# Kernel optimization log

Measured on AMD Instinct MI355X. Metric: run time of the kernel, lower is better.

The kernel has to match this reference:

```python
import jax, jax.numpy as jnp
import numpy as np

R_DIM, R2_DIM, MIX, IN_DIM, HID = 128, 64, 32, 512, 256
B, T = 256, 16
MAX_ITER = 12
LR_R, LR_R2 = 0.1, 0.1
LMDA_R, LMDA_R2 = 0.01, 0.01
SPAT_W, TEMP_W = 1.0, 1.0
LN_EPS = 1e-6


def _soft_thresh(r, lmda):
    # non-negative proximal L1 step, as in the source soft_thresholding
    return jax.nn.relu(jnp.abs(r) - lmda) * jnp.sign(r)


def setup_inputs() -> dict:
    key = jax.random.key(0)
    ks = jax.random.split(key, 8)

    def xavier(k, shape):
        std = (2.0 / (shape[0] + shape[-1])) ** 0.5
        return std * jax.random.normal(k, shape, dtype=jnp.float32)

    return {
        'X': jax.random.normal(ks[0], (B, T, IN_DIM), dtype=jnp.float32),
        'dec_W': xavier(ks[1], (R_DIM, IN_DIM)),
        'dec_b': jnp.zeros((IN_DIM,), jnp.float32),
        'temporal': xavier(ks[2], (MIX, R_DIM * R_DIM)),
        'h1_W': xavier(ks[3], (R2_DIM, HID)),
        'h1_b': jnp.zeros((HID,), jnp.float32),
        'ln_s': jnp.ones((HID,), jnp.float32),
        'ln_b': jnp.zeros((HID,), jnp.float32),
        'h2_W': xavier(ks[4], (HID, HID)),
        'h2_b': jnp.zeros((HID,), jnp.float32),
        'h3_W': xavier(ks[5], (HID, MIX)),
        'h3_b': jnp.zeros((MIX,), jnp.float32),
    }


def _hypernet(r2, h1_W, h1_b, ln_s, ln_b, h2_W, h2_b, h3_W, h3_b):
    x = r2 @ h1_W + h1_b
    mu = jnp.mean(x, axis=-1, keepdims=True)
    var = jnp.var(x, axis=-1, keepdims=True)
    x = (x - mu) * jax.lax.rsqrt(var + LN_EPS) * ln_s + ln_b  # LayerNorm
    x = jax.nn.elu(x)
    x = x @ h2_W + h2_b
    x = x @ h3_W + h3_b
    return jax.nn.relu(x)  # mixture weights w: (B, MIX)


def _forward(X, dec_W, dec_b, temporal, h1_W, h1_b, ln_s, ln_b, h2_W, h2_b, h3_W, h3_b):
    hp = (h1_W, h1_b, ln_s, ln_b, h2_W, h2_b, h3_W, h3_b)
    Vk = temporal.reshape(MIX, R_DIM, R_DIM)

    def decode(r):
        return r @ dec_W + dec_b  # linear spatial decoder (MSE branch)

    def temp_pred(r_prev, r2):
        w = _hypernet(r2, *hp)                       # (B, MIX)
        V = jnp.einsum('bm,mij->bij', w, Vk)         # (B, R, R)
        return jnp.einsum('bij,bj->bi', V, r_prev)   # r_hat: (B, R)

    def time_step(carry, x_t):
        r_prev, r2 = carry

        def energy(r, r2_):
            r_hat = temp_pred(r_prev, r2_)
            spat = jnp.sum((decode(r) - x_t) ** 2)
            temp = jnp.sum((r - r_hat) ** 2)
            return SPAT_W * spat + TEMP_W * temp

        grad_fn = jax.grad(energy, argnums=(0, 1))

        def ista(c, _):
            r, r2_ = c
            gr, gr2 = grad_fn(r, r2_)
            r = _soft_thresh(r - LR_R * gr, LR_R * LMDA_R)
            r2_ = _soft_thresh(r2_ - LR_R2 * gr2, LR_R2 * LMDA_R2)
            return (r, r2_), None

        r0 = temp_pred(r_prev, r2)  # warm start from temporal prediction
        (r, r2), _ = jax.lax.scan(ista, (r0, r2), None, length=MAX_ITER)

        r_hat = temp_pred(r_prev, r2)
        spat_rhat = jnp.mean(jnp.sum((decode(r_hat) - x_t) ** 2, axis=-1))
        spat_rbar = jnp.mean(jnp.sum((decode(r) - x_t) ** 2, axis=-1))
        temp_loss = jnp.mean(jnp.sum((r - r_hat) ** 2, axis=-1))
        return (r, r2), jnp.stack([spat_rhat, spat_rbar, temp_loss])

    r_init = jnp.zeros((X.shape[0], R_DIM), X.dtype)
    r2_init = jnp.zeros((X.shape[0], R2_DIM), X.dtype)
    (r_fin, r2_fin), losses = jax.lax.scan(
        time_step, (r_init, r2_init), jnp.swapaxes(X, 0, 1))
    return jnp.mean(losses, axis=0), r_fin, r2_fin


def reference(X, dec_W, dec_b, temporal, h1_W, h1_b, ln_s, ln_b, h2_W, h2_b, h3_W, h3_b):
    return _forward(X, dec_W, dec_b, temporal, h1_W, h1_b, ln_s, ln_b,
                    h2_W, h2_b, h3_W, h3_b)
```

## Files before the change

kernel.cpp:

```cpp
#include <hip/hip_runtime.h>
#include <cstdint>
#include <cstddef>

#define R_DIM   128
#define R2_DIM  64
#define MIX     32
#define IN_DIM  512
#define HID     256
#define B_SZ    256
#define T_SZ    16
#define MAX_IT  12

#define OFF_G    0
#define OFF_U    24576
#define OFF_SX   548864
#define OFF_FLAG 552960
#define OFF_LOSS 552961

__device__ __forceinline__ float softt(float v, float lam) {
  float a = fabsf(v) - lam;
  return a > 0.f ? (v > 0.f ? a : -a) : 0.f;
}

__device__ __forceinline__ float rdlane(float v, int lane) {
  int i = __builtin_amdgcn_readlane(__float_as_int(v), lane);
  return __int_as_float(i);
}

__device__ __forceinline__ float wsum_all(float v) {
#pragma unroll
  for (int off = 32; off; off >>= 1) v += __shfl_xor(v, off, 64);
  return v;
}

__device__ __forceinline__ float wsum(float v) {
#pragma unroll
  for (int off = 32; off; off >>= 1) v += __shfl_down(v, off, 64);
  return v;
}

__device__ __forceinline__ float pairsum32(float pm) {
  float a = pm, b = pm;
  asm volatile("v_permlane32_swap_b32 %0, %1" : "+v"(a), "+v"(b));
  return a + b;
}

__device__ void ensure_c_dev(int l, const float* __restrict__ T2, float* cS,
                             int* cstL, const float* rpL) {
  if (cstL[0]) return;
  for (int p = l; p < MIX * R_DIM; p += 64) {
    const float* row = T2 + (size_t)p * R_DIM;
    float acc = 0.f;
    for (int j4 = 0; j4 < R_DIM / 4; j4++) {
      float4 w4 = *(const float4*)(row + j4 * 4);
      float4 r4 = *(const float4*)(rpL + j4 * 4);
      acc += w4.x * r4.x + w4.y * r4.y + w4.z * r4.z + w4.w * r4.w;
    }
    cS[(p >> 7) * 129 + (p & 127)] = acc;
  }
  if (l == 0) cstL[0] = 1;
}

__device__ __noinline__ float2 rhat_cold(int l, const float* __restrict__ T2,
                                         float* cS, int* cstL,
                                         const float* rpL, const float* wL) {
  ensure_c_dev(l, T2, cS, cstL, rpL);
  float a0 = 0.f, a1 = 0.f;
#pragma unroll
  for (int m4 = 0; m4 < 8; m4++) {
    float4 w4 = *(const float4*)&wL[m4 * 4];
    int mb = m4 * 4;
    a0 += w4.x * cS[(mb + 0) * 129 + l] + w4.y * cS[(mb + 1) * 129 + l] +
          w4.z * cS[(mb + 2) * 129 + l] + w4.w * cS[(mb + 3) * 129 + l];
    a1 += w4.x * cS[(mb + 0) * 129 + 64 + l] + w4.y * cS[(mb + 1) * 129 + 64 + l] +
          w4.z * cS[(mb + 2) * 129 + 64 + l] + w4.w * cS[(mb + 3) * 129 + 64 + l];
  }
  return make_float2(a0, a1);
}

__device__ __noinline__ int hyp_fwd_cold(
    int l, float r2v, int zr2,
    const float* __restrict__ h1W, const float* __restrict__ h1b,
    const float* __restrict__ lns, const float* __restrict__ lnb,
    const float* __restrict__ h2W, const float* __restrict__ h2b,
    const float* __restrict__ h3W, const float* __restrict__ h3b,
    float* aL, float* xhL, float* x2L, float* wL, float* rstdL) {
  float x1[4];
#pragma unroll
  for (int q = 0; q < 4; q++) x1[q] = h1b[l + 64 * q];
  if (!zr2) {
    for (int k = 0; k < R2_DIM; k++) {
      float rk = rdlane(r2v, k);
      if (rk != 0.f) {
#pragma unroll
        for (int q = 0; q < 4; q++) x1[q] += rk * h1W[k * HID + l + 64 * q];
      }
    }
  }
  float s1 = x1[0] + x1[1] + x1[2] + x1[3];
  float s2 = x1[0] * x1[0] + x1[1] * x1[1] + x1[2] * x1[2] + x1[3] * x1[3];
  s1 = wsum_all(s1); s2 = wsum_all(s2);
  float mu = s1 * (1.f / HID);
  float var = s2 * (1.f / HID) - mu * mu;
  float rstd = rsqrtf(var + 1e-6f);
  if (l == 0) rstdL[0] = rstd;
  bool anz = false;
#pragma unroll
  for (int q = 0; q < 4; q++) {
    float xh = (x1[q] - mu) * rstd;
    xhL[l + 64 * q] = xh;
    float y = xh * lns[l + 64 * q] + lnb[l + 64 * q];
    float a = (y > 0.f) ? y : expm1f(y);
    aL[l + 64 * q] = a;
    anz |= (a != 0.f);
  }
  bool za = (__ballot(anz) == 0ull);
  float x2[4];
#pragma unroll
  for (int q = 0; q < 4; q++) x2[q] = h2b[l + 64 * q];
  if (!za) {
    for (int k4 = 0; k4 < HID / 4; k4++) {
      float4 a4 = *(const float4*)&aL[k4 * 4];
#pragma unroll
      for (int c = 0; c < 4; c++) {
        float ac = (&a4.x)[c];
        int k = k4 * 4 + c;
#pragma unroll
        for (int q = 0; q < 4; q++) x2[q] += ac * h2W[(size_t)k * HID + l + 64 * q];
      }
    }
  }
  bool x2nz = false;
#pragma unroll
  for (int q = 0; q < 4; q++) { x2L[l + 64 * q] = x2[q]; x2nz |= (x2[q] != 0.f); }
  bool zx2 = (__ballot(x2nz) == 0ull);
  int m = l & 31, kh = l >> 5;
  float p = 0.f;
  if (!zx2) {
    for (int kk = 0; kk < 128; kk++) {
      int k = kh * 128 + kk;
      p += x2L[k] * h3W[k * MIX + m];
    }
  }
  p += __shfl_xor(p, 32, 64);
  float wv = 0.f;
  if (l < 32) { wv = fmaxf(h3b[l] + p, 0.f); wL[l] = wv; }
  return (__ballot(wv != 0.f) == 0ull) ? 1 : 0;
}

__device__ __noinline__ float2 hyp_bwd_cold(
    int l, float r2v, int zw,
    const float* __restrict__ T2,
    const float* __restrict__ h1W, const float* __restrict__ lns,
    const float* __restrict__ h2W, const float* __restrict__ h3W,
    float* cS, int* cstL, const float* rpL, const float* eL,
    const float* aL, const float* xhL, const float* wL,
    float* dx3L, float* dx2L, float* dx1L, const float* rstdL) {
  bool zd3 = true;
  if (!zw) {
    ensure_c_dev(l, T2, cS, cstL, rpL);
    int m = l & 31, ih = l >> 5;
    float p = 0.f;
    for (int ii = 0; ii < 64; ii++) {
      int i = ih * 64 + ii;
      p += eL[i] * cS[m * 129 + i];
    }
    p += __shfl_xor(p, 32, 64);
    float d3 = 0.f;
    if (l < 32) { d3 = (wL[l] > 0.f) ? (-2.f * p) : 0.f; dx3L[l] = d3; }
    zd3 = (__ballot(d3 != 0.f) == 0ull);
  }
  float g = 0.f;
  if (!zd3) {
    float rstd = rstdL[0];
    float dx2[4] = {0.f, 0.f, 0.f, 0.f};
#pragma unroll
    for (int m4 = 0; m4 < 8; m4++) {
      float4 d4 = *(const float4*)&dx3L[m4 * 4];
#pragma unroll
      for (int q = 0; q < 4; q++) {
        const float* r3 = h3W + (size_t)(l + 64 * q) * MIX + m4 * 4;
        dx2[q] += d4.x * r3[0] + d4.y * r3[1] + d4.z * r3[2] + d4.w * r3[3];
      }
    }
#pragma unroll
    for (int q = 0; q < 4; q++) dx2L[l + 64 * q] = dx2[q];
    float dxh[4];
    float s1 = 0.f, s2 = 0.f;
#pragma unroll
    for (int q = 0; q < 4; q++) {
      float da = 0.f;
      const float* row = h2W + (size_t)(l + 64 * q) * HID;
      for (int k4 = 0; k4 < HID / 4; k4++) {
        float4 w4 = *(const float4*)(row + k4 * 4);
        float4 d4 = *(const float4*)&dx2L[k4 * 4];
        da += w4.x * d4.x + w4.y * d4.y + w4.z * d4.z + w4.w * d4.w;
      }
      float a = aL[l + 64 * q];
      float dy = da * (a > 0.f ? 1.f : (a + 1.f));
      dxh[q] = dy * lns[l + 64 * q];
      s1 += dxh[q]; s2 += dxh[q] * xhL[l + 64 * q];
    }
    s1 = wsum_all(s1); s2 = wsum_all(s2);
#pragma unroll
    for (int q = 0; q < 4; q++) {
      float dx1 = rstd * (dxh[q] - s1 * (1.f / HID) - xhL[l + 64 * q] * (s2 * (1.f / HID)));
      dx1L[l + 64 * q] = dx1;
    }
    const float* row1 = h1W + (size_t)l * HID;
    for (int j4 = 0; j4 < HID / 4; j4++) {
      float4 w4 = *(const float4*)(row1 + j4 * 4);
      float4 d4 = *(const float4*)&dx1L[j4 * 4];
      g += w4.x * d4.x + w4.y * d4.y + w4.z * d4.z + w4.w * d4.w;
    }
  }
  float r2n = softt(r2v - 0.1f * g, 0.001f);
  int fl = 0;
  if (__ballot(r2n != r2v) != 0ull) fl |= 1;
  if (__ballot(r2n != 0.f) == 0ull) fl |= 2;
  return make_float2(r2n, __int_as_float(fl));
}

__global__ __launch_bounds__(256) void k_prep(const float* __restrict__ X,
                                              const float* __restrict__ decb,
                                              const float* __restrict__ decW,
                                              const float* __restrict__ h1W,
                                              const float* __restrict__ h1b,
                                              const float* __restrict__ lns,
                                              const float* __restrict__ lnb,
                                              const float* __restrict__ h2W,
                                              const float* __restrict__ h2b,
                                              const float* __restrict__ h3W,
                                              const float* __restrict__ h3b,
                                              float* __restrict__ ws,
                                              float* __restrict__ out) {
  __shared__ __align__(16) float As[8][IN_DIM];
  __shared__ float Wsp[128][65];
  __shared__ float scr[256];
  __shared__ __align__(16) float aF[HID], xhF[HID], x2F[HID];
  __shared__ __align__(16) float wF[MIX];
  __shared__ float rsF[1];
  float* G = ws + OFF_G;
  float* U = ws + OFF_U;
  float* SX = ws + OFF_SX;
  const int tid = threadIdx.x;
  const int bx = blockIdx.x;

  if (bx == 528) {
    if (tid < 64) {
      int z = hyp_fwd_cold(tid, 0.f, 1, h1W, h1b, lns, lnb, h2W, h2b, h3W, h3b,
                           aF, xhF, x2F, wF, rsF);
      if (tid == 0) ((int*)(ws + OFF_FLAG))[0] = z;
    }
    return;
  }
  const bool isG = (bx >= 512);

  if (bx == 0 && tid < 3) out[tid] = 0.f;
  if (bx == 0 && tid < 48) ws[OFF_LOSS + tid] = 0.f;

  {
    int g = tid >> 5;
    int f0 = tid & 31;
    if (!isG) {
      int row0 = bx * 8;
      float p = 0.f;
#pragma unroll
      for (int q = 0; q < 4; q++) {
        int f4 = f0 + 32 * q;
        float4 xv = *reinterpret_cast<const float4*>(X + (size_t)(row0 + g) * IN_DIM + f4 * 4);
        float4 bv = *reinterpret_cast<const float4*>(decb + f4 * 4);
        float4 v = make_float4(xv.x - bv.x, xv.y - bv.y, xv.z - bv.z, xv.w - bv.w);
        *reinterpret_cast<float4*>(&As[g][f4 * 4]) = v;
        p += v.x * v.x + v.y * v.y + v.z * v.z + v.w * v.w;
      }
      scr[tid] = p;
    } else {
      int row0 = (bx - 512) * 8;
#pragma unroll
      for (int q = 0; q < 4; q++) {
        int f4 = f0 + 32 * q;
        float4 v = *reinterpret_cast<const float4*>(decW + (size_t)(row0 + g) * IN_DIM + f4 * 4);
        *reinterpret_cast<float4*>(&As[g][f4 * 4]) = v;
      }
    }
  }
  __syncthreads();
  if (!isG && tid < 8) {
    float s = 0.f;
#pragma unroll
    for (int q = 0; q < 32; q++) s += scr[tid * 32 + q];
    SX[bx * 8 + tid] = s;
  }

  const int j = tid & 127;
  const int gh = tid >> 7;
  float acc[4] = {0.f, 0.f, 0.f, 0.f};

  for (int kp = 0; kp < 8; kp++) {
    __syncthreads();
#pragma unroll
    for (int pass = 0; pass < 8; pass++) {
      int row = pass * 16 + (tid >> 4);
      int kk = (tid & 15) * 4;
      float4 v = *reinterpret_cast<const float4*>(decW + (size_t)row * IN_DIM + kp * 64 + kk);
      Wsp[row][kk + 0] = v.x; Wsp[row][kk + 1] = v.y;
      Wsp[row][kk + 2] = v.z; Wsp[row][kk + 3] = v.w;
    }
    __syncthreads();
    float wreg[64];
#pragma unroll
    for (int kk = 0; kk < 64; kk++) wreg[kk] = Wsp[j][kk];
#pragma unroll
    for (int gi = 0; gi < 4; gi++) {
      int gg = gh * 4 + gi;
      float a = acc[gi];
#pragma unroll
      for (int k4 = 0; k4 < 16; k4++) {
        float4 a4 = *reinterpret_cast<const float4*>(&As[gg][kp * 64 + k4 * 4]);
        a += a4.x * wreg[k4 * 4 + 0] + a4.y * wreg[k4 * 4 + 1] +
             a4.z * wreg[k4 * 4 + 2] + a4.w * wreg[k4 * 4 + 3];
      }
      acc[gi] = a;
    }
  }

  if (!isG) {
    int row0 = bx * 8;
#pragma unroll
    for (int gi = 0; gi < 4; gi++)
      U[(size_t)(row0 + gh * 4 + gi) * R_DIM + j] = acc[gi];
  } else {
    int row0 = (bx - 512) * 8;
#pragma unroll
    for (int gi = 0; gi < 4; gi++) {
      int rr = row0 + gh * 4 + gi;
      float gv = -0.2f * acc[gi];
      if (rr == j) gv += 0.8f;
      G[(size_t)rr * R_DIM + j] = gv;
    }
  }
}

__global__ __launch_bounds__(256, 4) void k_ista(float* __restrict__ ws,
                                                 float* __restrict__ out) {
  if (((const int*)(ws + OFF_FLAG))[0] == 0) return;
  __shared__ __align__(16) float rbuf[2][R_DIM];
  __shared__ float scr[8];

  const int tid = threadIdx.x;
  const int w = tid >> 6;
  const int l6 = tid & 63;
  const int i = (w << 5) + (l6 & 31);
  const int kh = l6 >> 5;
  const int bt = blockIdx.x;
  const int b = bt >> 4;
  const int t = bt & 15;
  const float* Gg = ws + OFF_G;
  const float* Ug = ws + OFF_U;

  float Ga[64];
#pragma unroll
  for (int kk = 0; kk < 64; kk++)
    Ga[kk] = Gg[(size_t)(kh * 64 + kk) * R_DIM + i];

  const float u = Ug[(size_t)bt * R_DIM + i];
  const float u02 = 0.2f * u;

  auto mvhalf = [&](const float* vptr) {
    const float* vp = vptr + (kh << 6);
    float p0 = 0.f, p1 = 0.f, p2 = 0.f, p3 = 0.f;
#pragma unroll
    for (int k4 = 0; k4 < 16; k4++) {
      float4 v4 = *reinterpret_cast<const float4*>(vp + k4 * 4);
      p0 += v4.x * Ga[k4 * 4 + 0];
      p1 += v4.y * Ga[k4 * 4 + 1];
      p2 += v4.z * Ga[k4 * 4 + 2];
      p3 += v4.w * Ga[k4 * 4 + 3];
    }
    float pm = (p0 + p1) + (p2 + p3);
    return pairsum32(pm);
  };

  float r = softt(u02, 0.001f);
  if (kh == 0) rbuf[1][i] = r;
  __syncthreads();
#pragma unroll 1
  for (int it = 1; it < MAX_IT; it++) {
    float mv = mvhalf(rbuf[it & 1]);
    r = softt(mv + u02, 0.001f);
    if (kh == 0) rbuf[(it & 1) ^ 1][i] = r;
    __syncthreads();
  }
  float mvf = mvhalf(rbuf[0]);
  float gb = 0.8f * r - mvf;
  float l1 = (kh == 0) ? (r * (5.f * gb) - 2.f * r * u) : 0.f;
  float l2 = (kh == 0) ? (r * r) : 0.f;
  l1 = wsum(l1); l2 = wsum(l2);
  if (l6 == 0) { scr[w * 2 + 0] = l1; scr[w * 2 + 1] = l2; }
  __syncthreads();
  if (tid == 0) {
    float s1 = scr[0] + scr[2] + scr[4] + scr[6];
    float s2 = scr[1] + scr[3] + scr[5] + scr[7];
    float sx = ws[OFF_SX + bt];
    float* loss = ws + OFF_LOSS;
    atomicAdd(&loss[0 * 16 + t], sx);
    atomicAdd(&loss[1 * 16 + t], s1 + sx);
    atomicAdd(&loss[2 * 16 + t], s2);
  }
  if (t == T_SZ - 1 && kh == 0) out[3 + b * R_DIM + i] = r;
  if (t == 0 && w == 0) out[3 + B_SZ * R_DIM + b * R2_DIM + l6] = 0.f;
}

__global__ void k_fin(const float* __restrict__ ws, float* __restrict__ out) {
  if (((const int*)(ws + OFF_FLAG))[0] == 0) return;
  int k = threadIdx.x;
  if (k < 3) {
    float s = 0.f;
#pragma unroll
    for (int t = 0; t < 16; t++) s += ws[OFF_LOSS + k * 16 + t];
    out[k] = s * (1.f / (B_SZ * T_SZ));
  }
}

__global__ __launch_bounds__(256, 1) void k_main(
    float* __restrict__ ws, const float* __restrict__ T2,
    const float* __restrict__ h1W, const float* __restrict__ h1b,
    const float* __restrict__ lns, const float* __restrict__ lnb,
    const float* __restrict__ h2W, const float* __restrict__ h2b,
    const float* __restrict__ h3W, const float* __restrict__ h3b,
    float* __restrict__ out) {
  if (((const int*)(ws + OFF_FLAG))[0] != 0) return;
  __shared__ __align__(16) float rbuf[2][R_DIM];
  __shared__ __align__(16) float rhL[R_DIM];
  __shared__ __align__(16) float cS[MIX * 129];
  __shared__ __align__(16) float aL[HID];
  __shared__ __align__(16) float xhL[HID];
  __shared__ __align__(16) float x2L[HID];
  __shared__ __align__(16) float dx1L[HID];
  __shared__ __align__(16) float dx2L[HID];
  __shared__ __align__(16) float wL[MIX];
  __shared__ __align__(16) float dx3L[MIX];
  __shared__ __align__(16) float eL[R_DIM];
  __shared__ __align__(16) float rpL[R_DIM];
  __shared__ float rstdL[1];
  __shared__ int cstL[1];
  __shared__ int flagL[1];

  const int tid = threadIdx.x;
  const int w = tid >> 6;
  const int l6 = tid & 63;
  const int i = (w << 5) + (l6 & 31);
  const int kh = l6 >> 5;
  const int b = blockIdx.x;
  const float* Gg = ws + OFF_G;
  const float* Ug = ws + OFF_U;
  const float* SXg = ws + OFF_SX;

  float r2v = 0.f;
  bool zr2 = true, rhv;

  if (w == 0) {
    int z = hyp_fwd_cold(l6, 0.f, 1, h1W, h1b, lns, lnb, h2W, h2b, h3W, h3b,
                         aL, xhL, x2L, wL, rstdL);
    if (l6 == 0) flagL[0] = z;
  }
  __syncthreads();
  bool zw = flagL[0] != 0;

  float Ga[64];
#pragma unroll
  for (int kk = 0; kk < 64; kk++)
    Ga[kk] = Gg[(size_t)(kh * 64 + kk) * R_DIM + i];

  float rOwn = 0.f;
  float lc0 = 0.f, lc1 = 0.f, lc2 = 0.f, sxa = 0.f;

  auto mvhalf = [&](const float* vptr) {
    const float* vp = vptr + (kh << 6);
    float p0 = 0.f, p1 = 0.f, p2 = 0.f, p3 = 0.f;
#pragma unroll
    for (int k4 = 0; k4 < 16; k4++) {
      float4 v4 = *reinterpret_cast<const float4*>(vp + k4 * 4);
      p0 += v4.x * Ga[k4 * 4 + 0];
      p1 += v4.y * Ga[k4 * 4 + 1];
      p2 += v4.z * Ga[k4 * 4 + 2];
      p3 += v4.w * Ga[k4 * 4 + 3];
    }
    float pm = (p0 + p1) + (p2 + p3);
    return pm + __shfl_xor(pm, 32, 64);
  };

  float rh_own = 0.f;
  auto refresh_rh = [&]() {
    if (zw) { rh_own = 0.f; return; }
    __syncthreads();
    if (w == 0) {
      float2 rr = rhat_cold(l6, T2, cS, cstL, rpL, wL);
      rhL[l6] = rr.x; rhL[64 + l6] = rr.y;
    }
    __syncthreads();
    rh_own = rhL[i];
  };

  float un = Ug[(size_t)(b * T_SZ) * R_DIM + i];
  float sxn = SXg[b * T_SZ];

#pragma unroll 1
  for (int t = 0; t < T_SZ; t++) {
    float u = un, sxv = sxn;
    if (t < T_SZ - 1) {
      un = Ug[(size_t)(b * T_SZ + t + 1) * R_DIM + i];
      sxn = SXg[b * T_SZ + t + 1];
    }
    float u02 = 0.2f * u;
    if (kh == 0) rpL[i] = rOwn;
    if (tid == 0) cstL[0] = 0;
    refresh_rh();
    rhv = true;
    rOwn = rh_own;
    __syncthreads();
    if (kh == 0) rbuf[0][i] = rOwn;
    __syncthreads();
    bool rzero = zw;
#pragma unroll 1
    for (int it = 0; it < MAX_IT; it++) {
      if (!rhv) { refresh_rh(); rhv = true; }
      float mv = 0.f;
      if (!rzero) mv = mvhalf(rbuf[it & 1]);
      rzero = false;
      float rNew = softt(mv + 0.2f * rh_own + u02, 0.001f);
      if (kh == 0) {
        eL[i] = rOwn - rh_own;
        rbuf[(it & 1) ^ 1][i] = rNew;
      }
      rOwn = rNew;
      __syncthreads();
      if (!(zw && zr2)) {
        if (w == 0) {
          float2 br = hyp_bwd_cold(l6, r2v, zw ? 1 : 0, T2, h1W, lns, h2W, h3W,
                                   cS, cstL, rpL, eL, aL, xhL, wL,
                                   dx3L, dx2L, dx1L, rstdL);
          r2v = br.x;
          if (l6 == 0) flagL[0] = __float_as_int(br.y);
        }
        __syncthreads();
        int fl = flagL[0];
        zr2 = (fl & 2) != 0;
        if (fl & 1) {
          if (w == 0) {
            int z = hyp_fwd_cold(l6, r2v, zr2 ? 1 : 0, h1W, h1b, lns, lnb,
                                 h2W, h2b, h3W, h3b, aL, xhL, x2L, wL, rstdL);
            if (l6 == 0) flagL[0] = z;
          }
          __syncthreads();
          zw = flagL[0] != 0;
          rhv = false;
        }
      }
    }
    if (!rhv) { refresh_rh(); rhv = true; }
    {
      float mv = mvhalf(rbuf[MAX_IT & 1]);
      float gb = 0.8f * rOwn - mv;
      if (kh == 0) lc1 += rOwn * (5.f * gb) - 2.f * rOwn * u;
      if (zw) {
        if (kh == 0) lc2 += rOwn * rOwn;
      } else {
        float mvh = mvhalf(rhL);
        float gh = 0.8f * rh_own - mvh;
        if (kh == 0) {
          lc0 += rh_own * (5.f * gh) - 2.f * rh_own * u;
          float d = rOwn - rh_own;
          lc2 += d * d;
        }
      }
      if (tid == 0) sxa += sxv;
    }
  }

  const float inv = 1.f / (B_SZ * T_SZ);
  float t0 = wsum(lc0), t1 = wsum(lc1), t2 = wsum(lc2);
  if (l6 == 0) {
    float s = (w == 0) ? sxa : 0.f;
    atomicAdd(&out[0], (t0 + s) * inv);
    atomicAdd(&out[1], (t1 + s) * inv);
    atomicAdd(&out[2], t2 * inv);
  }
  if (kh == 0) out[3 + b * R_DIM + i] = rOwn;
  if (w == 0) out[3 + B_SZ * R_DIM + b * R2_DIM + l6] = r2v;
}

extern "C" void kernel_launch(void* const* d_in, const int* in_sizes, int n_in,
                              void* d_out, int out_size, void* d_ws, size_t ws_size,
                              hipStream_t stream) {
  const float* X = (const float*)d_in[0];
  const float* decW = (const float*)d_in[1];
  const float* decb = (const float*)d_in[2];
  const float* temporal = (const float*)d_in[3];
  const float* h1W = (const float*)d_in[4];
  const float* h1b = (const float*)d_in[5];
  const float* lns = (const float*)d_in[6];
  const float* lnb = (const float*)d_in[7];
  const float* h2W = (const float*)d_in[8];
  const float* h2b = (const float*)d_in[9];
  const float* h3W = (const float*)d_in[10];
  const float* h3b = (const float*)d_in[11];
  float* ws = (float*)d_ws;
  float* out = (float*)d_out;

  k_prep<<<529, 256, 0, stream>>>(X, decb, decW, h1W, h1b, lns, lnb,
                                  h2W, h2b, h3W, h3b, ws, out);
  k_main<<<B_SZ, 256, 0, stream>>>(ws, temporal, h1W, h1b, lns, lnb,
                                   h2W, h2b, h3W, h3b, out);
  k_ista<<<B_SZ * T_SZ, 256, 0, stream>>>(ws, out);
  k_fin<<<1, 64, 0, stream>>>(ws, out);
}
```

Before: 202.0 us.

## Process two (b,t) problems per ISTA block with each lane holding two G columns

The ISTA kernel now handles two batch-time problems per block, and each thread keeps two 64-element slices of the G matrix in registers. All 64 lanes of a wave now produce a useful output, where before only half did after the pair reduction. This removes the idle half-lanes in the final stage and halves the number of blocks and G reloads. In exchange, register use per thread doubles (128 floats for G), so the launch bound is lowered to 2 waves per SIMD, which reduces occupancy.

```diff
diff --git a/kernel.cpp b/kernel.cpp
--- a/kernel.cpp
+++ b/kernel.cpp
@@ -342,74 +342,81 @@
   }
 }
 
-__global__ __launch_bounds__(256, 4) void k_ista(float* __restrict__ ws,
+__global__ __launch_bounds__(256, 2) void k_ista(float* __restrict__ ws,
                                                  float* __restrict__ out) {
   if (((const int*)(ws + OFF_FLAG))[0] == 0) return;
-  __shared__ __align__(16) float rbuf[2][R_DIM];
+  __shared__ __align__(16) float rbuf[2][2][R_DIM];
   __shared__ float scr[8];
 
   const int tid = threadIdx.x;
-  const int w = tid >> 6;
+  const int half = tid >> 7;
+  const int wv = tid >> 6;
+  const int wbt = wv & 1;
   const int l6 = tid & 63;
-  const int i = (w << 5) + (l6 & 31);
+  const int p = (wbt << 5) + (l6 & 31);
   const int kh = l6 >> 5;
-  const int bt = blockIdx.x;
+  const int iown = p + (kh << 6);
+  const int bt = blockIdx.x * 2 + half;
   const int b = bt >> 4;
   const int t = bt & 15;
   const float* Gg = ws + OFF_G;
   const float* Ug = ws + OFF_U;
 
-  float Ga[64];
-#pragma unroll
-  for (int kk = 0; kk < 64; kk++)
-    Ga[kk] = Gg[(size_t)(kh * 64 + kk) * R_DIM + i];
-
-  const float u = Ug[(size_t)bt * R_DIM + i];
+  float Ga0[64], Ga1[64];
+#pragma unroll
+  for (int kk = 0; kk < 64; kk++) {
+    const float* row = Gg + (size_t)(kh * 64 + kk) * R_DIM;
+    Ga0[kk] = row[p];
+    Ga1[kk] = row[p + 64];
+  }
+
+  const float u = Ug[(size_t)bt * R_DIM + iown];
   const float u02 = 0.2f * u;
 
-  auto mvhalf = [&](const float* vptr) {
-    const float* vp = vptr + (kh << 6);
-    float p0 = 0.f, p1 = 0.f, p2 = 0.f, p3 = 0.f;
+  auto mvown = [&](const float* vbase) {
+    const float* vp = vbase + (kh << 6);
+    float s0a = 0.f, s0b = 0.f, s1a = 0.f, s1b = 0.f;
 #pragma unroll
     for (int k4 = 0; k4 < 16; k4++) {
       float4 v4 = *reinterpret_cast<const float4*>(vp + k4 * 4);
-      p0 += v4.x * Ga[k4 * 4 + 0];
-      p1 += v4.y * Ga[k4 * 4 + 1];
-      p2 += v4.z * Ga[k4 * 4 + 2];
-      p3 += v4.w * Ga[k4 * 4 + 3];
-    }
-    float pm = (p0 + p1) + (p2 + p3);
-    return pairsum32(pm);
+      s0a += v4.x * Ga0[k4 * 4 + 0] + v4.y * Ga0[k4 * 4 + 1];
+      s0b += v4.z * Ga0[k4 * 4 + 2] + v4.w * Ga0[k4 * 4 + 3];
+      s1a += v4.x * Ga1[k4 * 4 + 0] + v4.y * Ga1[k4 * 4 + 1];
+      s1b += v4.z * Ga1[k4 * 4 + 2] + v4.w * Ga1[k4 * 4 + 3];
+    }
+    float mv0 = pairsum32(s0a + s0b);
+    float mv1 = pairsum32(s1a + s1b);
+    return kh ? mv1 : mv0;
   };
 
   float r = softt(u02, 0.001f);
-  if (kh == 0) rbuf[1][i] = r;
+  rbuf[half][1][iown] = r;
   __syncthreads();
 #pragma unroll 1
   for (int it = 1; it < MAX_IT; it++) {
-    float mv = mvhalf(rbuf[it & 1]);
+    float mv = mvown(&rbuf[half][it & 1][0]);
     r = softt(mv + u02, 0.001f);
-    if (kh == 0) rbuf[(it & 1) ^ 1][i] = r;
+    rbuf[half][(it & 1) ^ 1][iown] = r;
     __syncthreads();
   }
-  float mvf = mvhalf(rbuf[0]);
+  float mvf = mvown(&rbuf[half][0][0]);
   float gb = 0.8f * r - mvf;
-  float l1 = (kh == 0) ? (r * (5.f * gb) - 2.f * r * u) : 0.f;
-  float l2 = (kh == 0) ? (r * r) : 0.f;
+  float l1 = r * (5.f * gb) - 2.f * r * u;
+  float l2 = r * r;
   l1 = wsum(l1); l2 = wsum(l2);
-  if (l6 == 0) { scr[w * 2 + 0] = l1; scr[w * 2 + 1] = l2; }
+  if (l6 == 0) { scr[wv * 2 + 0] = l1; scr[wv * 2 + 1] = l2; }
   __syncthreads();
-  if (tid == 0) {
-    float s1 = scr[0] + scr[2] + scr[4] + scr[6];
-    float s2 = scr[1] + scr[3] + scr[5] + scr[7];
+  if ((tid & 127) == 0) {
+    float s1 = scr[half * 4 + 0] + scr[half * 4 + 2];
+    float s2 = scr[half * 4 + 1] + scr[half * 4 + 3];
     float sx = ws[OFF_SX + bt];
     float* loss = ws + OFF_LOSS;
     atomicAdd(&loss[0 * 16 + t], sx);
     atomicAdd(&loss[1 * 16 + t], s1 + sx);
     atomicAdd(&loss[2 * 16 + t], s2);
   }
-  if (t == T_SZ - 1 && kh == 0) out[3 + b * R_DIM + i] = r;
-  if (t == 0 && w == 0) out[3 + B_SZ * R_DIM + b * R2_DIM + l6] = 0.f;
+  if (t == T_SZ - 1) out[3 + b * R_DIM + iown] = r;
+  if (t == 0 && wbt == 0) out[3 + B_SZ * R_DIM + b * R2_DIM + l6] = 0.f;
 }
 
 __global__ void k_fin(const float* __restrict__ ws, float* __restrict__ out) {
@@ -613,6 +620,6 @@
                                   h2W, h2b, h3W, h3b, ws, out);
   k_main<<<B_SZ, 256, 0, stream>>>(ws, temporal, h1W, h1b, lns, lnb,
                                    h2W, h2b, h3W, h3b, out);
-  k_ista<<<B_SZ * T_SZ, 256, 0, stream>>>(ws, out);
+  k_ista<<<B_SZ * T_SZ / 2, 256, 0, stream>>>(ws, out);
   k_fin<<<1, 64, 0, stream>>>(ws, out);
 }
```

Measured after the change: 207.9 us. +2.9%, slower.

## Fold final loss reduction into k_ista and stream decW directly in prep GEMM

Applied to the files above, without the earlier changes.

Removes the separate k_fin launch: the last k_ista block, found with a global atomic counter after a threadfence, sums the per-timestep losses and writes the outputs. The prep GEMM no longer stages decW tiles through padded shared memory with two barriers per tile; each thread instead reads its decW row with float4 global loads. An empty asm barrier pins the G coefficients in registers in k_ista. This saves one kernel launch and the shared-memory staging and syncs, in exchange for uncoalesced row-strided global loads and an atomic counter.

```diff
diff --git a/kernel.cpp b/kernel.cpp
--- a/kernel.cpp
+++ b/kernel.cpp
@@ -16,6 +16,7 @@
 #define OFF_SX   548864
 #define OFF_FLAG 552960
 #define OFF_LOSS 552961
+#define OFF_CNT  553012
 
 __device__ __forceinline__ float softt(float v, float lam) {
   float a = fabsf(v) - lam;
@@ -235,7 +236,6 @@
                                               float* __restrict__ ws,
                                               float* __restrict__ out) {
   __shared__ __align__(16) float As[8][IN_DIM];
-  __shared__ float Wsp[128][65];
   __shared__ float scr[256];
   __shared__ __align__(16) float aF[HID], xhF[HID], x2F[HID];
   __shared__ __align__(16) float wF[MIX];
@@ -258,6 +258,7 @@
 
   if (bx == 0 && tid < 3) out[tid] = 0.f;
   if (bx == 0 && tid < 48) ws[OFF_LOSS + tid] = 0.f;
+  if (bx == 0 && tid == 48) ((int*)(ws + OFF_CNT))[0] = 0;
 
   {
     int g = tid >> 5;
@@ -296,32 +297,15 @@
   const int j = tid & 127;
   const int gh = tid >> 7;
   float acc[4] = {0.f, 0.f, 0.f, 0.f};
-
-  for (int kp = 0; kp < 8; kp++) {
-    __syncthreads();
-#pragma unroll
-    for (int pass = 0; pass < 8; pass++) {
-      int row = pass * 16 + (tid >> 4);
-      int kk = (tid & 15) * 4;
-      float4 v = *reinterpret_cast<const float4*>(decW + (size_t)row * IN_DIM + kp * 64 + kk);
-      Wsp[row][kk + 0] = v.x; Wsp[row][kk + 1] = v.y;
-      Wsp[row][kk + 2] = v.z; Wsp[row][kk + 3] = v.w;
-    }
-    __syncthreads();
-    float wreg[64];
-#pragma unroll
-    for (int kk = 0; kk < 64; kk++) wreg[kk] = Wsp[j][kk];
+  const float* wrow = decW + (size_t)j * IN_DIM;
+
+#pragma unroll 4
+  for (int k4 = 0; k4 < IN_DIM / 4; k4++) {
+    float4 w4 = *reinterpret_cast<const float4*>(wrow + k4 * 4);
 #pragma unroll
     for (int gi = 0; gi < 4; gi++) {
-      int gg = gh * 4 + gi;
-      float a = acc[gi];
-#pragma unroll
-      for (int k4 = 0; k4 < 16; k4++) {
-        float4 a4 = *reinterpret_cast<const float4*>(&As[gg][kp * 64 + k4 * 4]);
-        a += a4.x * wreg[k4 * 4 + 0] + a4.y * wreg[k4 * 4 + 1] +
-             a4.z * wreg[k4 * 4 + 2] + a4.w * wreg[k4 * 4 + 3];
-      }
-      acc[gi] = a;
+      float4 a4 = *reinterpret_cast<const float4*>(&As[gh * 4 + gi][k4 * 4]);
+      acc[gi] += w4.x * a4.x + w4.y * a4.y + w4.z * a4.z + w4.w * a4.w;
     }
   }
 
@@ -363,6 +347,9 @@
 #pragma unroll
   for (int kk = 0; kk < 64; kk++)
     Ga[kk] = Gg[(size_t)(kh * 64 + kk) * R_DIM + i];
+#pragma unroll
+  for (int kk = 0; kk < 64; kk++)
+    asm volatile("" : "+v"(Ga[kk]));
 
   const float u = Ug[(size_t)bt * R_DIM + i];
   const float u02 = 0.2f * u;
@@ -407,20 +394,20 @@
     atomicAdd(&loss[0 * 16 + t], sx);
     atomicAdd(&loss[1 * 16 + t], s1 + sx);
     atomicAdd(&loss[2 * 16 + t], s2);
+    __threadfence();
+    int old = atomicAdd((int*)(ws + OFF_CNT), 1);
+    if (old == B_SZ * T_SZ - 1) {
+      float s[3] = {0.f, 0.f, 0.f};
+#pragma unroll
+      for (int k = 0; k < 3; k++)
+        for (int tt = 0; tt < 16; tt++)
+          s[k] += atomicAdd(&loss[k * 16 + tt], 0.f);
+      const float inv = 1.f / (B_SZ * T_SZ);
+      out[0] = s[0] * inv; out[1] = s[1] * inv; out[2] = s[2] * inv;
+    }
   }
   if (t == T_SZ - 1 && kh == 0) out[3 + b * R_DIM + i] = r;
   if (t == 0 && w == 0) out[3 + B_SZ * R_DIM + b * R2_DIM + l6] = 0.f;
-}
-
-__global__ void k_fin(const float* __restrict__ ws, float* __restrict__ out) {
-  if (((const int*)(ws + OFF_FLAG))[0] == 0) return;
-  int k = threadIdx.x;
-  if (k < 3) {
-    float s = 0.f;
-#pragma unroll
-    for (int t = 0; t < 16; t++) s += ws[OFF_LOSS + k * 16 + t];
-    out[k] = s * (1.f / (B_SZ * T_SZ));
-  }
 }
 
 __global__ __launch_bounds__(256, 1) void k_main(
@@ -614,5 +601,4 @@
   k_main<<<B_SZ, 256, 0, stream>>>(ws, temporal, h1W, h1b, lns, lnb,
                                    h2W, h2b, h3W, h3b, out);
   k_ista<<<B_SZ * T_SZ, 256, 0, stream>>>(ws, out);
-  k_fin<<<1, 64, 0, stream>>>(ws, out);
-}
+}
```

Measured after the change: 258.6 us. 28.0% more time.
